# Kernel optimization log

Measured on AMD Instinct MI355X. Metric: run time of the kernel, lower is better.

The kernel has to match this reference:

```python
import jax, jax.numpy as jnp
import numpy as np

NUM_SEQS = 32
NUM_HEADS = 32
NUM_KV_HEADS = 8
HEAD_DIM = 128
BLOCK_SIZE = 16
MAX_CTX = 2048
BLOCKS_PER_SEQ = MAX_CTX // BLOCK_SIZE  # 128
NUM_BLOCKS = NUM_SEQS * BLOCKS_PER_SEQ  # 4096
SCALE = 1.0 / np.sqrt(HEAD_DIM)
ROPE_BASE = 10000.0


def setup_inputs() -> dict:
    key = jax.random.key(0)
    ks = jax.random.split(key, 8)
    q = jax.random.normal(ks[0], (NUM_SEQS, NUM_HEADS, HEAD_DIM), dtype=jnp.float32)
    k = jax.random.normal(ks[1], (NUM_SEQS, NUM_KV_HEADS, HEAD_DIM), dtype=jnp.float32)
    v = jax.random.normal(ks[2], (NUM_SEQS, NUM_KV_HEADS, HEAD_DIM), dtype=jnp.float32)
    # context length per request (>=1, <=MAX_CTX); new token sits at position ctx_len-1
    context_lens = jax.random.randint(ks[3], (NUM_SEQS,), 1, MAX_CTX + 1).astype(jnp.int32)
    position = context_lens - 1
    # each sequence owns a contiguous range of blocks (paged layout is arbitrary; this is a valid table)
    block_tables = jnp.arange(NUM_BLOCKS, dtype=jnp.int32).reshape(NUM_SEQS, BLOCKS_PER_SEQ)
    slot_mapping = (jnp.arange(NUM_SEQS, dtype=jnp.int32) * MAX_CTX + position).astype(jnp.int32)
    k_cache = jax.random.normal(ks[4], (NUM_BLOCKS, BLOCK_SIZE, NUM_KV_HEADS, HEAD_DIM), dtype=jnp.float32)
    v_cache = jax.random.normal(ks[5], (NUM_BLOCKS, BLOCK_SIZE, NUM_KV_HEADS, HEAD_DIM), dtype=jnp.float32)
    # standard neox RoPE tables
    inv_freq = 1.0 / (ROPE_BASE ** (jnp.arange(0, HEAD_DIM, 2, dtype=jnp.float32) / HEAD_DIM))
    t = jnp.arange(MAX_CTX, dtype=jnp.float32)
    freqs = jnp.outer(t, inv_freq)  # [MAX_CTX, HEAD_DIM//2]
    cos_cache = jnp.cos(freqs)
    sin_cache = jnp.sin(freqs)
    return {"q": q, "k": k, "v": v, "k_cache": k_cache, "v_cache": v_cache,
            "cos_cache": cos_cache, "sin_cache": sin_cache, "position": position,
            "slot_mapping": slot_mapping, "block_tables": block_tables,
            "context_lens": context_lens}


def _rope_neox(x, cos, sin):
    # x: [S, H, D], cos/sin: [S, D//2] -> broadcast over heads
    d2 = x.shape[-1] // 2
    x1, x2 = x[..., :d2], x[..., d2:]
    c, s = cos[:, None, :], sin[:, None, :]
    return jnp.concatenate([x1 * c - x2 * s, x2 * c + x1 * s], axis=-1)


def reference(q, k, v, k_cache, v_cache, cos_cache, sin_cache,
              position, slot_mapping, block_tables, context_lens):
    # 1) fused RoPE on q/k at the current position (decode step)
    cos = cos_cache[position]
    sin = sin_cache[position]
    q = _rope_neox(q, cos, sin)
    k = _rope_neox(k, cos, sin)
    # 2) reshape_and_cache: scatter new k/v into the paged caches at slot_mapping
    blk = slot_mapping // BLOCK_SIZE
    off = slot_mapping % BLOCK_SIZE
    k_cache = k_cache.at[blk, off].set(k)
    v_cache = v_cache.at[blk, off].set(v)
    # 3) paged decode attention: gather per-seq KV via block tables
    # [S, BLOCKS_PER_SEQ, BLOCK_SIZE, KVH, D] -> [S, MAX_CTX, KVH, D]
    k_seq = k_cache[block_tables].reshape(NUM_SEQS, MAX_CTX, NUM_KV_HEADS, HEAD_DIM)
    v_seq = v_cache[block_tables].reshape(NUM_SEQS, MAX_CTX, NUM_KV_HEADS, HEAD_DIM)
    group = NUM_HEADS // NUM_KV_HEADS
    qg = q.reshape(NUM_SEQS, NUM_KV_HEADS, group, HEAD_DIM)
    scores = jnp.einsum('skgd,stkd->skgt', qg, k_seq) * SCALE  # [S, KVH, G, T]
    valid = jnp.arange(MAX_CTX, dtype=jnp.int32)[None, :] < context_lens[:, None]  # [S, T]
    scores = jnp.where(valid[:, None, None, :], scores, jnp.float32(-1e30))
    p = jax.nn.softmax(scores, axis=-1)
    o = jnp.einsum('skgt,stkd->skgd', p, v_seq)
    return o.reshape(NUM_SEQS, NUM_HEADS * HEAD_DIM)
```

## Files before the change

### kernel.cpp

```cpp
#include <hip/hip_runtime.h>

#define NSEQ 32
#define NH 32
#define NKV 8
#define GRP 4
#define HD 128
#define BS 16
#define MAXCTX 2048
#define BPS 128
#define CHUNK 256
#define NSPLIT (MAXCTX / CHUNK)
#define SCALE 0.08838834764831845f

__device__ __forceinline__ float dot8(float4 qa, float4 qb, float4 ka, float4 kb) {
  float r = qa.x * ka.x;
  r = fmaf(qa.y, ka.y, r);
  r = fmaf(qa.z, ka.z, r);
  r = fmaf(qa.w, ka.w, r);
  r = fmaf(qb.x, kb.x, r);
  r = fmaf(qb.y, kb.y, r);
  r = fmaf(qb.z, kb.z, r);
  r = fmaf(qb.w, kb.w, r);
  return r;
}

__device__ __forceinline__ float red16(float x) {
  x += __shfl_xor(x, 1);
  x += __shfl_xor(x, 2);
  x += __shfl_xor(x, 4);
  x += __shfl_xor(x, 8);
  return x;
}

__device__ __forceinline__ void red_sub(float4& v) {
  v.x += __shfl_xor(v.x, 16); v.y += __shfl_xor(v.y, 16);
  v.z += __shfl_xor(v.z, 16); v.w += __shfl_xor(v.w, 16);
  v.x += __shfl_xor(v.x, 32); v.y += __shfl_xor(v.y, 32);
  v.z += __shfl_xor(v.z, 32); v.w += __shfl_xor(v.w, 32);
}

extern "C" __global__ __launch_bounds__(256, 8)
void paged_split(const float* __restrict__ q,
                 const float* __restrict__ k_new,
                 const float* __restrict__ v_new,
                 const float* __restrict__ k_cache,
                 const float* __restrict__ v_cache,
                 const float* __restrict__ cos_cache,
                 const float* __restrict__ sin_cache,
                 const int* __restrict__ block_tables,
                 const int* __restrict__ context_lens,
                 float* __restrict__ accW,
                 float2* __restrict__ mlW)
{
  const int kv = blockIdx.x;
  int s = -1, sp = blockIdx.y;
  for (int i = 0; i < NSEQ; ++i) {
    int ns = (context_lens[i] + CHUNK - 1) / CHUNK;
    if (sp < ns) { s = i; break; }
    sp -= ns;
  }
  if (s < 0) return;

  const int ctx = context_lens[s];
  const int t0  = sp * CHUNK;
  const int tend = min(t0 + CHUNK, ctx);
  const int ntok = tend - t0;
  const int pos  = ctx - 1;
  const bool has_new = (pos >= t0) && (pos < tend);
  const int ncache = has_new ? (pos - t0) : ntok;

  const int tid  = threadIdx.x;
  const int lane = tid & 63;
  const int w    = tid >> 6;
  const int sub  = lane >> 4;
  const int li   = lane & 15;

  __shared__ float cs_lds[64];
  __shared__ float sn_lds[64];
  __shared__ float qrot[GRP * HD];
  __shared__ float krot[HD];
  __shared__ int   bt[CHUNK / BS];
  __shared__ float s_sc[GRP][CHUNK];
  __shared__ float acc_lds[4][GRP][HD];

  if (tid < 64) {
    cs_lds[tid] = cos_cache[pos * 64 + tid];
    sn_lds[tid] = sin_cache[pos * 64 + tid];
  }
  if (tid >= 192 && tid < 192 + CHUNK / BS)
    bt[tid - 192] = block_tables[s * BPS + (t0 >> 4) + (tid - 192)];
  __syncthreads();

  {
    const float* qp = q + (s * NH + kv * GRP) * HD;
#pragma unroll
    for (int j = tid; j < GRP * HD; j += 256) {
      int h = j >> 7, d = j & 127;
      float r;
      if (d < 64) r = qp[h * HD + d] * cs_lds[d] - qp[h * HD + d + 64] * sn_lds[d];
      else        r = qp[h * HD + d] * cs_lds[d - 64] + qp[h * HD + d - 64] * sn_lds[d - 64];
      qrot[j] = r * SCALE;
    }
  }
  if (has_new && tid < 128) {
    const float* kp = k_new + (s * NKV + kv) * HD;
    int d = tid;
    float r;
    if (d < 64) r = kp[d] * cs_lds[d] - kp[d + 64] * sn_lds[d];
    else        r = kp[d] * cs_lds[d - 64] + kp[d - 64] * sn_lds[d - 64];
    krot[d] = r;
  }
  __syncthreads();

  float4 qf0[GRP], qf1[GRP];
#pragma unroll
  for (int h = 0; h < GRP; ++h) {
    qf0[h] = *(const float4*)&qrot[h * HD + li * 4];
    qf1[h] = *(const float4*)&qrot[h * HD + 64 + li * 4];
  }

  if (w == 0 && has_new) {
    float4 ka = *(const float4*)&krot[li * 4];
    float4 kb = *(const float4*)&krot[64 + li * 4];
    float p0 = red16(dot8(qf0[0], qf1[0], ka, kb));
    float p1 = red16(dot8(qf0[1], qf1[1], ka, kb));
    float p2 = red16(dot8(qf0[2], qf1[2], ka, kb));
    float p3 = red16(dot8(qf0[3], qf1[3], ka, kb));
    if (lane == 0) {
      s_sc[0][ncache] = p0; s_sc[1][ncache] = p1;
      s_sc[2][ncache] = p2; s_sc[3][ncache] = p3;
    }
  }

  {
    const int c = li & 3;
    for (int j0 = w * 4; j0 < ncache; j0 += 16) {
      int j = j0 + sub;
      int jc = j < ncache ? j : (ncache - 1);
      int blk = bt[jc >> 4];
      int a = ((blk * BS + (jc & 15)) * NKV + kv) * HD + li * 4;
      float4 ka = *(const float4*)&k_cache[a];
      float4 kb = *(const float4*)&k_cache[a + 64];
      float p0 = dot8(qf0[0], qf1[0], ka, kb);
      float p1 = dot8(qf0[1], qf1[1], ka, kb);
      float p2 = dot8(qf0[2], qf1[2], ka, kb);
      float p3 = dot8(qf0[3], qf1[3], ka, kb);
      p0 += __shfl_xor(p0, 1); p1 += __shfl_xor(p1, 1);
      p2 += __shfl_xor(p2, 1); p3 += __shfl_xor(p3, 1);
      p0 += __shfl_xor(p0, 2); p1 += __shfl_xor(p1, 2);
      p2 += __shfl_xor(p2, 2); p3 += __shfl_xor(p3, 2);
      float x = (c == 0) ? p0 : (c == 1) ? p1 : (c == 2) ? p2 : p3;
      x += __shfl_xor(x, 4);
      x += __shfl_xor(x, 8);
      if (li < 4 && j < ncache) s_sc[li][j] = x;
    }
  }
  __syncthreads();

  {
    float m = -3.0e38f;
    for (int t = lane; t < ntok; t += 64) m = fmaxf(m, s_sc[w][t]);
#pragma unroll
    for (int msk = 1; msk < 64; msk <<= 1) m = fmaxf(m, __shfl_xor(m, msk));
    float sum = 0.f;
    for (int t = lane; t < ntok; t += 64) {
      float p = __expf(s_sc[w][t] - m);
      s_sc[w][t] = p;
      sum += p;
    }
#pragma unroll
    for (int msk = 1; msk < 64; msk <<= 1) sum += __shfl_xor(sum, msk);
    if (lane == 0) {
      int part = ((s * NKV + kv) * GRP + w) * NSPLIT + sp;
      mlW[part] = make_float2(m, sum);
    }
  }
  __syncthreads();

  float4 aa0 = {0,0,0,0}, aa1 = {0,0,0,0}, aa2 = {0,0,0,0}, aa3 = {0,0,0,0};
  float4 ab0 = {0,0,0,0}, ab1 = {0,0,0,0}, ab2 = {0,0,0,0}, ab3 = {0,0,0,0};
  for (int j0 = w * 4; j0 < ncache; j0 += 16) {
    int j = j0 + sub;
    int jc = j < ncache ? j : (ncache - 1);
    int blk = bt[jc >> 4];
    int a = ((blk * BS + (jc & 15)) * NKV + kv) * HD + li * 4;
    float4 va = *(const float4*)&v_cache[a];
    float4 vb = *(const float4*)&v_cache[a + 64];
    bool valid = j < ncache;
    float p0 = valid ? s_sc[0][j] : 0.f;
    float p1 = valid ? s_sc[1][j] : 0.f;
    float p2 = valid ? s_sc[2][j] : 0.f;
    float p3 = valid ? s_sc[3][j] : 0.f;
    aa0.x = fmaf(p0, va.x, aa0.x); aa0.y = fmaf(p0, va.y, aa0.y);
    aa0.z = fmaf(p0, va.z, aa0.z); aa0.w = fmaf(p0, va.w, aa0.w);
    ab0.x = fmaf(p0, vb.x, ab0.x); ab0.y = fmaf(p0, vb.y, ab0.y);
    ab0.z = fmaf(p0, vb.z, ab0.z); ab0.w = fmaf(p0, vb.w, ab0.w);
    aa1.x = fmaf(p1, va.x, aa1.x); aa1.y = fmaf(p1, va.y, aa1.y);
    aa1.z = fmaf(p1, va.z, aa1.z); aa1.w = fmaf(p1, va.w, aa1.w);
    ab1.x = fmaf(p1, vb.x, ab1.x); ab1.y = fmaf(p1, vb.y, ab1.y);
    ab1.z = fmaf(p1, vb.z, ab1.z); ab1.w = fmaf(p1, vb.w, ab1.w);
    aa2.x = fmaf(p2, va.x, aa2.x); aa2.y = fmaf(p2, va.y, aa2.y);
    aa2.z = fmaf(p2, va.z, aa2.z); aa2.w = fmaf(p2, va.w, aa2.w);
    ab2.x = fmaf(p2, vb.x, ab2.x); ab2.y = fmaf(p2, vb.y, ab2.y);
    ab2.z = fmaf(p2, vb.z, ab2.z); ab2.w = fmaf(p2, vb.w, ab2.w);
    aa3.x = fmaf(p3, va.x, aa3.x); aa3.y = fmaf(p3, va.y, aa3.y);
    aa3.z = fmaf(p3, va.z, aa3.z); aa3.w = fmaf(p3, va.w, aa3.w);
    ab3.x = fmaf(p3, vb.x, ab3.x); ab3.y = fmaf(p3, vb.y, ab3.y);
    ab3.z = fmaf(p3, vb.z, ab3.z); ab3.w = fmaf(p3, vb.w, ab3.w);
  }
  red_sub(aa0); red_sub(aa1); red_sub(aa2); red_sub(aa3);
  red_sub(ab0); red_sub(ab1); red_sub(ab2); red_sub(ab3);
  if (lane < 16) {
    *(float4*)&acc_lds[w][0][li * 4] = aa0;
    *(float4*)&acc_lds[w][1][li * 4] = aa1;
    *(float4*)&acc_lds[w][2][li * 4] = aa2;
    *(float4*)&acc_lds[w][3][li * 4] = aa3;
    *(float4*)&acc_lds[w][0][64 + li * 4] = ab0;
    *(float4*)&acc_lds[w][1][64 + li * 4] = ab1;
    *(float4*)&acc_lds[w][2][64 + li * 4] = ab2;
    *(float4*)&acc_lds[w][3][64 + li * 4] = ab3;
  }
  __syncthreads();

  {
    const float* vp = v_new + (s * NKV + kv) * HD;
#pragma unroll
    for (int j = tid; j < GRP * HD; j += 256) {
      int h = j >> 7, d = j & 127;
      float o = acc_lds[0][h][d] + acc_lds[1][h][d] + acc_lds[2][h][d] + acc_lds[3][h][d];
      if (has_new) o = fmaf(s_sc[h][ncache], vp[d], o);
      int part = ((s * NKV + kv) * GRP + h) * NSPLIT + sp;
      accW[part * HD + d] = o;
    }
  }
}

extern "C" __global__ __launch_bounds__(256, 8)
void paged_reduce(const float* __restrict__ accW,
                  const float2* __restrict__ mlW,
                  const int* __restrict__ context_lens,
                  float* __restrict__ out)
{
  const int tid  = threadIdx.x;
  const int lane = tid & 63;
  const int w    = tid >> 6;
  const int idx  = blockIdx.x * 4 + w;
  const int s    = idx >> 5;
  const int h    = idx & 31;
  const int kv   = h >> 2, g = h & 3;
  const int ctx  = context_lens[s];
  const int nsp  = (ctx + CHUNK - 1) / CHUNK;
  const int pbase = ((s * NKV + kv) * GRP + g) * NSPLIT;

  float m = -3.0e38f;
  for (int i = 0; i < nsp; ++i) m = fmaxf(m, mlW[pbase + i].x);
  float L = 0.f;
  float2 acc = {0.f, 0.f};
  for (int i = 0; i < nsp; ++i) {
    float2 ml = mlW[pbase + i];
    float sc = __expf(ml.x - m);
    L += ml.y * sc;
    float2 a = *(const float2*)&accW[(pbase + i) * HD + lane * 2];
    acc.x = fmaf(a.x, sc, acc.x);
    acc.y = fmaf(a.y, sc, acc.y);
  }
  float inv = 1.0f / L;
  float2 o = make_float2(acc.x * inv, acc.y * inv);
  *(float2*)&out[(s * NH + h) * HD + lane * 2] = o;
}

extern "C" void kernel_launch(void* const* d_in, const int* in_sizes, int n_in,
                              void* d_out, int out_size, void* d_ws, size_t ws_size,
                              hipStream_t stream) {
  const float* q         = (const float*)d_in[0];
  const float* k_new     = (const float*)d_in[1];
  const float* v_new     = (const float*)d_in[2];
  const float* k_cache   = (const float*)d_in[3];
  const float* v_cache   = (const float*)d_in[4];
  const float* cos_cache = (const float*)d_in[5];
  const float* sin_cache = (const float*)d_in[6];
  const int* block_tables = (const int*)d_in[9];
  const int* context_lens = (const int*)d_in[10];
  float* out = (float*)d_out;

  float*  accW = (float*)d_ws;
  float2* mlW  = (float2*)((char*)d_ws + (size_t)NSEQ * NKV * GRP * NSPLIT * HD * sizeof(float));

  dim3 grid(NKV, NSEQ * NSPLIT);
  paged_split<<<grid, 256, 0, stream>>>(q, k_new, v_new, k_cache, v_cache,
                                        cos_cache, sin_cache, block_tables,
                                        context_lens, accW, mlW);
  paged_reduce<<<NSEQ * NH / 4, 256, 0, stream>>>(accW, mlW, context_lens, out);
}
```

Measured before the change: 58.33 us.

## Fuse QK scoring and PV accumulation into single-pass online softmax per wave

Replaces the three-phase split kernel (score all tokens into LDS, block-wide softmax, then PV pass) with one loop per wave that loads K and V together and keeps a running max, sum and rescaled accumulator. Per-wave partial max/sum are combined across the four waves and with the new token at the end, then written out. This removes the score LDS buffer and two block barriers and lets K and V loads overlap. In exchange it adds per-iteration shuffle reductions, exp rescaling and more registers, so launch bounds drop from 8 to 4 blocks per CU, which lowers occupancy.

```diff
diff --git a/kernel.cpp b/kernel.cpp
--- a/kernel.cpp
+++ b/kernel.cpp
@@ -11,6 +11,7 @@
 #define CHUNK 256
 #define NSPLIT (MAXCTX / CHUNK)
 #define SCALE 0.08838834764831845f
+#define NEGINF -3.0e38f
 
 __device__ __forceinline__ float dot8(float4 qa, float4 qb, float4 ka, float4 kb) {
   float r = qa.x * ka.x;
@@ -39,7 +40,7 @@
   v.z += __shfl_xor(v.z, 32); v.w += __shfl_xor(v.w, 32);
 }
 
-extern "C" __global__ __launch_bounds__(256, 8)
+extern "C" __global__ __launch_bounds__(256, 4)
 void paged_split(const float* __restrict__ q,
                  const float* __restrict__ k_new,
                  const float* __restrict__ v_new,
@@ -80,7 +81,9 @@
   __shared__ float qrot[GRP * HD];
   __shared__ float krot[HD];
   __shared__ int   bt[CHUNK / BS];
-  __shared__ float s_sc[GRP][CHUNK];
+  __shared__ float snew_lds[GRP];
+  __shared__ float m_lds[4][GRP];
+  __shared__ float l_lds[4][GRP];
   __shared__ float acc_lds[4][GRP][HD];
 
   if (tid < 64) {
@@ -127,70 +130,60 @@
     float p2 = red16(dot8(qf0[2], qf1[2], ka, kb));
     float p3 = red16(dot8(qf0[3], qf1[3], ka, kb));
     if (lane == 0) {
-      s_sc[0][ncache] = p0; s_sc[1][ncache] = p1;
-      s_sc[2][ncache] = p2; s_sc[3][ncache] = p3;
-    }
-  }
-
-  {
-    const int c = li & 3;
-    for (int j0 = w * 4; j0 < ncache; j0 += 16) {
-      int j = j0 + sub;
-      int jc = j < ncache ? j : (ncache - 1);
-      int blk = bt[jc >> 4];
-      int a = ((blk * BS + (jc & 15)) * NKV + kv) * HD + li * 4;
-      float4 ka = *(const float4*)&k_cache[a];
-      float4 kb = *(const float4*)&k_cache[a + 64];
-      float p0 = dot8(qf0[0], qf1[0], ka, kb);
-      float p1 = dot8(qf0[1], qf1[1], ka, kb);
-      float p2 = dot8(qf0[2], qf1[2], ka, kb);
-      float p3 = dot8(qf0[3], qf1[3], ka, kb);
-      p0 += __shfl_xor(p0, 1); p1 += __shfl_xor(p1, 1);
-      p2 += __shfl_xor(p2, 1); p3 += __shfl_xor(p3, 1);
-      p0 += __shfl_xor(p0, 2); p1 += __shfl_xor(p1, 2);
-      p2 += __shfl_xor(p2, 2); p3 += __shfl_xor(p3, 2);
-      float x = (c == 0) ? p0 : (c == 1) ? p1 : (c == 2) ? p2 : p3;
-      x += __shfl_xor(x, 4);
-      x += __shfl_xor(x, 8);
-      if (li < 4 && j < ncache) s_sc[li][j] = x;
-    }
-  }
-  __syncthreads();
-
-  {
-    float m = -3.0e38f;
-    for (int t = lane; t < ntok; t += 64) m = fmaxf(m, s_sc[w][t]);
-#pragma unroll
-    for (int msk = 1; msk < 64; msk <<= 1) m = fmaxf(m, __shfl_xor(m, msk));
-    float sum = 0.f;
-    for (int t = lane; t < ntok; t += 64) {
-      float p = __expf(s_sc[w][t] - m);
-      s_sc[w][t] = p;
-      sum += p;
-    }
-#pragma unroll
-    for (int msk = 1; msk < 64; msk <<= 1) sum += __shfl_xor(sum, msk);
-    if (lane == 0) {
-      int part = ((s * NKV + kv) * GRP + w) * NSPLIT + sp;
-      mlW[part] = make_float2(m, sum);
-    }
-  }
-  __syncthreads();
-
+      snew_lds[0] = p0; snew_lds[1] = p1;
+      snew_lds[2] = p2; snew_lds[3] = p3;
+    }
+  }
+
+  float m0 = NEGINF, m1 = NEGINF, m2 = NEGINF, m3 = NEGINF;
+  float l0 = 0.f, l1 = 0.f, l2 = 0.f, l3 = 0.f;
   float4 aa0 = {0,0,0,0}, aa1 = {0,0,0,0}, aa2 = {0,0,0,0}, aa3 = {0,0,0,0};
   float4 ab0 = {0,0,0,0}, ab1 = {0,0,0,0}, ab2 = {0,0,0,0}, ab3 = {0,0,0,0};
+
   for (int j0 = w * 4; j0 < ncache; j0 += 16) {
     int j = j0 + sub;
-    int jc = j < ncache ? j : (ncache - 1);
+    bool valid = j < ncache;
+    int jc = valid ? j : (ncache - 1);
     int blk = bt[jc >> 4];
     int a = ((blk * BS + (jc & 15)) * NKV + kv) * HD + li * 4;
+    float4 ka = *(const float4*)&k_cache[a];
+    float4 kb = *(const float4*)&k_cache[a + 64];
     float4 va = *(const float4*)&v_cache[a];
     float4 vb = *(const float4*)&v_cache[a + 64];
-    bool valid = j < ncache;
-    float p0 = valid ? s_sc[0][j] : 0.f;
-    float p1 = valid ? s_sc[1][j] : 0.f;
-    float p2 = valid ? s_sc[2][j] : 0.f;
-    float p3 = valid ? s_sc[3][j] : 0.f;
+
+    float s0 = red16(dot8(qf0[0], qf1[0], ka, kb));
+    float s1 = red16(dot8(qf0[1], qf1[1], ka, kb));
+    float s2 = red16(dot8(qf0[2], qf1[2], ka, kb));
+    float s3 = red16(dot8(qf0[3], qf1[3], ka, kb));
+    if (!valid) { s0 = NEGINF; s1 = NEGINF; s2 = NEGINF; s3 = NEGINF; }
+
+    float n0 = fmaxf(s0, __shfl_xor(s0, 16)); n0 = fmaxf(n0, __shfl_xor(n0, 32));
+    float n1 = fmaxf(s1, __shfl_xor(s1, 16)); n1 = fmaxf(n1, __shfl_xor(n1, 32));
+    float n2 = fmaxf(s2, __shfl_xor(s2, 16)); n2 = fmaxf(n2, __shfl_xor(n2, 32));
+    float n3 = fmaxf(s3, __shfl_xor(s3, 16)); n3 = fmaxf(n3, __shfl_xor(n3, 32));
+
+    if (n0 > m0 || n1 > m1 || n2 > m2 || n3 > m3) {
+      float t0_ = fmaxf(m0, n0), f0 = __expf(m0 - t0_); m0 = t0_;
+      float t1_ = fmaxf(m1, n1), f1 = __expf(m1 - t1_); m1 = t1_;
+      float t2_ = fmaxf(m2, n2), f2 = __expf(m2 - t2_); m2 = t2_;
+      float t3_ = fmaxf(m3, n3), f3 = __expf(m3 - t3_); m3 = t3_;
+      l0 *= f0; l1 *= f1; l2 *= f2; l3 *= f3;
+      aa0.x *= f0; aa0.y *= f0; aa0.z *= f0; aa0.w *= f0;
+      ab0.x *= f0; ab0.y *= f0; ab0.z *= f0; ab0.w *= f0;
+      aa1.x *= f1; aa1.y *= f1; aa1.z *= f1; aa1.w *= f1;
+      ab1.x *= f1; ab1.y *= f1; ab1.z *= f1; ab1.w *= f1;
+      aa2.x *= f2; aa2.y *= f2; aa2.z *= f2; aa2.w *= f2;
+      ab2.x *= f2; ab2.y *= f2; ab2.z *= f2; ab2.w *= f2;
+      aa3.x *= f3; aa3.y *= f3; aa3.z *= f3; aa3.w *= f3;
+      ab3.x *= f3; ab3.y *= f3; ab3.z *= f3; ab3.w *= f3;
+    }
+
+    float p0 = __expf(s0 - m0);
+    float p1 = __expf(s1 - m1);
+    float p2 = __expf(s2 - m2);
+    float p3 = __expf(s3 - m3);
+    l0 += p0; l1 += p1; l2 += p2; l3 += p3;
+
     aa0.x = fmaf(p0, va.x, aa0.x); aa0.y = fmaf(p0, va.y, aa0.y);
     aa0.z = fmaf(p0, va.z, aa0.z); aa0.w = fmaf(p0, va.w, aa0.w);
     ab0.x = fmaf(p0, vb.x, ab0.x); ab0.y = fmaf(p0, vb.y, ab0.y);
@@ -208,8 +201,14 @@
     ab3.x = fmaf(p3, vb.x, ab3.x); ab3.y = fmaf(p3, vb.y, ab3.y);
     ab3.z = fmaf(p3, vb.z, ab3.z); ab3.w = fmaf(p3, vb.w, ab3.w);
   }
+
   red_sub(aa0); red_sub(aa1); red_sub(aa2); red_sub(aa3);
   red_sub(ab0); red_sub(ab1); red_sub(ab2); red_sub(ab3);
+  l0 += __shfl_xor(l0, 16); l0 += __shfl_xor(l0, 32);
+  l1 += __shfl_xor(l1, 16); l1 += __shfl_xor(l1, 32);
+  l2 += __shfl_xor(l2, 16); l2 += __shfl_xor(l2, 32);
+  l3 += __shfl_xor(l3, 16); l3 += __shfl_xor(l3, 32);
+
   if (lane < 16) {
     *(float4*)&acc_lds[w][0][li * 4] = aa0;
     *(float4*)&acc_lds[w][1][li * 4] = aa1;
@@ -220,17 +219,39 @@
     *(float4*)&acc_lds[w][2][64 + li * 4] = ab2;
     *(float4*)&acc_lds[w][3][64 + li * 4] = ab3;
   }
+  if (lane == 0) {
+    m_lds[w][0] = m0; m_lds[w][1] = m1; m_lds[w][2] = m2; m_lds[w][3] = m3;
+    l_lds[w][0] = l0; l_lds[w][1] = l1; l_lds[w][2] = l2; l_lds[w][3] = l3;
+  }
   __syncthreads();
 
   {
     const float* vp = v_new + (s * NKV + kv) * HD;
 #pragma unroll
-    for (int j = tid; j < GRP * HD; j += 256) {
-      int h = j >> 7, d = j & 127;
-      float o = acc_lds[0][h][d] + acc_lds[1][h][d] + acc_lds[2][h][d] + acc_lds[3][h][d];
-      if (has_new) o = fmaf(s_sc[h][ncache], vp[d], o);
+    for (int jj = tid; jj < GRP * HD; jj += 256) {
+      int h = jj >> 7, d = jj & 127;
+      float mw0 = m_lds[0][h], mw1 = m_lds[1][h], mw2 = m_lds[2][h], mw3 = m_lds[3][h];
+      float ms = fmaxf(fmaxf(mw0, mw1), fmaxf(mw2, mw3));
+      if (has_new) ms = fmaxf(ms, snew_lds[h]);
+      float o = __expf(mw0 - ms) * acc_lds[0][h][d]
+              + __expf(mw1 - ms) * acc_lds[1][h][d]
+              + __expf(mw2 - ms) * acc_lds[2][h][d]
+              + __expf(mw3 - ms) * acc_lds[3][h][d];
+      if (has_new) o = fmaf(__expf(snew_lds[h] - ms), vp[d], o);
       int part = ((s * NKV + kv) * GRP + h) * NSPLIT + sp;
       accW[part * HD + d] = o;
+    }
+    if (tid < GRP) {
+      int h = tid;
+      float mw0 = m_lds[0][h], mw1 = m_lds[1][h], mw2 = m_lds[2][h], mw3 = m_lds[3][h];
+      float ms = fmaxf(fmaxf(mw0, mw1), fmaxf(mw2, mw3));
+      if (has_new) ms = fmaxf(ms, snew_lds[h]);
+      float L = __expf(mw0 - ms) * l_lds[0][h]
+              + __expf(mw1 - ms) * l_lds[1][h]
+              + __expf(mw2 - ms) * l_lds[2][h]
+              + __expf(mw3 - ms) * l_lds[3][h];
+      if (has_new) L += __expf(snew_lds[h] - ms);
+      mlW[((s * NKV + kv) * GRP + h) * NSPLIT + sp] = make_float2(ms, L);
     }
   }
 }
@@ -252,7 +273,7 @@
   const int nsp  = (ctx + CHUNK - 1) / CHUNK;
   const int pbase = ((s * NKV + kv) * GRP + g) * NSPLIT;
 
-  float m = -3.0e38f;
+  float m = NEGINF;
   for (int i = 0; i < nsp; ++i) m = fmaxf(m, mlW[pbase + i].x);
   float L = 0.f;
   float2 acc = {0.f, 0.f};
```

Result: slower. 67.80 us, median of 2 (+16.2%).
